# Optimization experiments

Hardware: AMD Instinct MI355X
Metric: run time of the kernel (lower is better)

The kernel has to match this reference:

```python
import jax, jax.numpy as jnp
import numpy as np

N_HEADS = 16


def setup_inputs() -> dict:
    key = jax.random.key(0)
    k1, k2, k3, k4 = jax.random.split(key, 4)
    b, s, d = 2, 2048, 1024
    x = jax.random.normal(k1, (b, s, d), dtype=jnp.float32)
    attn_B = jax.random.normal(k2, (b, N_HEADS, s, s), dtype=jnp.float32) * 0.02
    W_attn = jax.random.normal(k3, (d, 3 * d), dtype=jnp.float32) * (1.0 / np.sqrt(d))
    b_attn = jax.random.normal(k4, (3 * d,), dtype=jnp.float32) * 0.01
    return {"x": x, "attn_B": attn_B, "W_attn": W_attn, "b_attn": b_attn}


def reference(x, attn_B, W_attn, b_attn):
    b, s, d = x.shape
    h = N_HEADS
    hd = d // h
    qkv = x @ W_attn + b_attn                       # [b, s, 3d]
    Q, K, V = jnp.split(qkv, 3, axis=-1)
    # [b, s, d] -> [b, h, s, hd]
    Q = Q.reshape(b, s, h, hd).transpose(0, 2, 1, 3)
    K = K.reshape(b, s, h, hd).transpose(0, 2, 1, 3)
    V = V.reshape(b, s, h, hd).transpose(0, 2, 1, 3)
    scale = 1.0 / jnp.sqrt(jnp.asarray(hd, dtype=Q.dtype))
    scores = jnp.einsum("bhqk,bhsk->bhqs", Q, K) * scale   # [b, h, s, s]
    attn = jax.nn.softmax(scores, axis=-1) + attn_B          # post-softmax additive bias
    y = jnp.einsum("bhqs,bhsd->bhqd", attn, V)               # [b, h, s, hd]
    y = y.transpose(0, 2, 1, 3).reshape(b, s, d)
    return y
```

## Files before the change

### kernel.cpp

```cpp
#include <hip/hip_runtime.h>
#include <hip/hip_bf16.h>


typedef __attribute__((ext_vector_type(4))) float  f32x4;
typedef __attribute__((ext_vector_type(8))) short  bf16x8;
typedef __attribute__((ext_vector_type(4))) short  s16x4;
typedef __attribute__((ext_vector_type(4))) unsigned u32x4;

__device__ __forceinline__ short f2bf(float f) {
    __hip_bfloat16 h = __float2bfloat16(f);
    return __builtin_bit_cast(short, h);
}

__device__ __forceinline__ unsigned cvt_pk_bf16(float lo, float hi) {
    unsigned w;
    asm("v_cvt_pk_bf16_f32 %0, %1, %2" : "=v"(w) : "v"(lo), "v"(hi));
    return w;
}

__device__ __forceinline__ bf16x8 pack8(f32x4 a, f32x4 b) {
    u32x4 t = (u32x4){cvt_pk_bf16(a[0], a[1]), cvt_pk_bf16(a[2], a[3]),
                      cvt_pk_bf16(b[0], b[1]), cvt_pk_bf16(b[2], b[3])};
    return __builtin_bit_cast(bf16x8, t);
}

__device__ __forceinline__ void gll16(const short* g, short* l) {
    __builtin_amdgcn_global_load_lds(
        (const __attribute__((address_space(1))) void*)g,
        (__attribute__((address_space(3))) void*)l, 16, 0, 0);
}

__global__ void conv_x_kernel(const float* __restrict__ x, short* __restrict__ xb) {
    int idx = blockIdx.x * 256 + threadIdx.x;
    f32x4 v = *reinterpret_cast<const f32x4*>(x + (size_t)idx * 4);
    s16x4 o;
    o[0] = f2bf(v[0]); o[1] = f2bf(v[1]); o[2] = f2bf(v[2]); o[3] = f2bf(v[3]);
    *reinterpret_cast<s16x4*>(xb + (size_t)idx * 4) = o;
}

__global__ void wtrans_kernel(const float* __restrict__ W, short* __restrict__ Wt) {
    __shared__ float tile[64][65];
    int kb = blockIdx.x, nb = blockIdx.y;
    int t = threadIdx.x;
    int c4 = (t & 15) * 4;
    int r0 = t >> 4;
#pragma unroll
    for (int rr = 0; rr < 4; ++rr) {
        int kl = r0 + rr * 16;
        f32x4 v = *reinterpret_cast<const f32x4*>(W + (size_t)(kb * 64 + kl) * 3072 + nb * 64 + c4);
        tile[kl][c4 + 0] = v[0]; tile[kl][c4 + 1] = v[1];
        tile[kl][c4 + 2] = v[2]; tile[kl][c4 + 3] = v[3];
    }
    __syncthreads();
#pragma unroll
    for (int rr = 0; rr < 4; ++rr) {
        int nl = r0 + rr * 16;
        s16x4 o;
#pragma unroll
        for (int i = 0; i < 4; ++i) o[i] = f2bf(tile[c4 + i][nl]);
        *reinterpret_cast<s16x4*>(Wt + (size_t)(nb * 64 + nl) * 1024 + kb * 64 + c4) = o;
    }
}

__global__ __launch_bounds__(256) void qkv_gemm_kernel(
    const short* __restrict__ xb, const short* __restrict__ Wt,
    const float* __restrict__ bias,
    short* __restrict__ Qo, short* __restrict__ Ko, short* __restrict__ Vto)
{
    __shared__ short As[128 * 64];
    __shared__ short Bs[128 * 64];
    int tid = threadIdx.x;
    int wave = tid >> 6, lane = tid & 63, g = lane >> 4, lr = lane & 15;
    int wr = wave >> 1, wc = wave & 1;
    int bm = blockIdx.x, bn = blockIdx.y;

    f32x4 acc[4][4];
#pragma unroll
    for (int a = 0; a < 4; ++a)
#pragma unroll
        for (int b = 0; b < 4; ++b) acc[a][b] = (f32x4){0.f, 0.f, 0.f, 0.f};

    for (int k0 = 0; k0 < 1024; k0 += 64) {
#pragma unroll
        for (int j = 0; j < 4; ++j) {
            int c = j * 256 + tid;
            int row = c >> 3, cc = c & 7;
            int scc = (cc ^ (row & 7)) * 8;
            gll16(xb + (size_t)(bm * 128 + row) * 1024 + k0 + scc,
                  &As[(j * 256 + wave * 64) * 8]);
            gll16(Wt + (size_t)(bn * 128 + row) * 1024 + k0 + scc,
                  &Bs[(j * 256 + wave * 64) * 8]);
        }
        __syncthreads();

        bf16x8 af[2][4], bfr[2][4];
#pragma unroll
        for (int mt = 0; mt < 4; ++mt) {
            int row = wr * 64 + mt * 16 + lr;
            af[0][mt] = *reinterpret_cast<const bf16x8*>(&As[row * 64 + (((g    ) ^ (lr & 7)) * 8)]);
            af[1][mt] = *reinterpret_cast<const bf16x8*>(&As[row * 64 + (((g + 4) ^ (lr & 7)) * 8)]);
        }
#pragma unroll
        for (int nt = 0; nt < 4; ++nt) {
            int row = wc * 64 + nt * 16 + lr;
            bfr[0][nt] = *reinterpret_cast<const bf16x8*>(&Bs[row * 64 + (((g    ) ^ (lr & 7)) * 8)]);
            bfr[1][nt] = *reinterpret_cast<const bf16x8*>(&Bs[row * 64 + (((g + 4) ^ (lr & 7)) * 8)]);
        }
#pragma unroll
        for (int mt = 0; mt < 4; ++mt)
#pragma unroll
            for (int nt = 0; nt < 4; ++nt) {
                acc[mt][nt] = __builtin_amdgcn_mfma_f32_16x16x32_bf16(af[0][mt], bfr[0][nt], acc[mt][nt], 0, 0, 0);
                acc[mt][nt] = __builtin_amdgcn_mfma_f32_16x16x32_bf16(af[1][mt], bfr[1][nt], acc[mt][nt], 0, 0, 0);
            }
        __syncthreads();
    }

#pragma unroll
    for (int nt = 0; nt < 4; ++nt) {
        int n = bn * 128 + wc * 64 + nt * 16 + lr;
        float bv = bias[n];
        int which = n >> 10;
        int h = (n >> 6) & 15;
        int dd = n & 63;
#pragma unroll
        for (int mt = 0; mt < 4; ++mt) {
            int m0 = bm * 128 + wr * 64 + mt * 16 + g * 4;
            int bb = m0 >> 11, s0 = m0 & 2047;
            if (which == 2) {
                s16x4 o;
#pragma unroll
                for (int r = 0; r < 4; ++r) o[r] = f2bf(acc[mt][nt][r] + bv);
                *reinterpret_cast<s16x4*>(
                    Vto + ((size_t)(bb * 16 + h) * 64 + dd) * 2048 + s0) = o;
            } else {
                short* base = (which == 0) ? Qo : Ko;
#pragma unroll
                for (int r = 0; r < 4; ++r)
                    base[(((size_t)bb * 16 + h) * 2048 + s0 + r) * 64 + dd] =
                        f2bf(acc[mt][nt][r] + bv);
            }
        }
    }
}

__global__ __launch_bounds__(512, 4) void attn_kernel(
    const short* __restrict__ Qw, const short* __restrict__ Kw, const short* __restrict__ Vtw,
    const float* __restrict__ attnB, float* __restrict__ out)
{
    __shared__ short Ks [2][64 * 64];
    __shared__ short Vts[2][64 * 64];
    __shared__ short Ps [8][16 * 64];

    int id = blockIdx.x;
    int bh3 = id & 7;
    int qt  = (id >> 3) & 15;
    int bh  = ((id >> 7) << 3) | bh3;
    int b = bh >> 4, h = bh & 15;
    int tid = threadIdx.x;
    int wave = tid >> 6, lane = tid & 63, g = lane >> 4, lr = lane & 15;

    const short* Qb = Qw  + (size_t)bh * 2048 * 64;
    const short* Kb = Kw  + (size_t)bh * 2048 * 64;
    const short* Vb = Vtw + (size_t)bh * 64 * 2048;
    const float* Bp = attnB + (size_t)bh * 2048 * 2048;

    int qbase = qt * 128 + wave * 16;

    bf16x8 qf0, qf1;
    {
        const short* qp = Qb + (size_t)(qbase + lr) * 64 + g * 8;
        qf0 = *reinterpret_cast<const bf16x8*>(qp);
        qf1 = *reinterpret_cast<const bf16x8*>(qp + 32);
    }
    const float* brow = Bp + (size_t)(qbase + lr) * 2048 + g * 8;

    f32x4 Os[4], Ob[4];
#pragma unroll
    for (int dt = 0; dt < 4; ++dt) { Os[dt] = (f32x4){0.f,0.f,0.f,0.f}; Ob[dt] = (f32x4){0.f,0.f,0.f,0.f}; }
    float lsum = 0.f;

#define STAGE_KV(buf, ktt) do {                                                   \
    int row = tid >> 3, cc = tid & 7;                                             \
    int scc = (cc ^ (row & 7)) * 8;                                               \
    gll16(Kb + (size_t)((ktt) * 64 + row) * 64 + scc,                             \
          &Ks[buf][wave * 512]);                                                  \
    gll16(Vb + (size_t)row * 2048 + (ktt) * 64 + scc,                             \
          &Vts[buf][wave * 512]);                                                 \
} while (0)

#define LOADB(d0, d1, d2, d3, ktt) do {                                           \
    const float* bp_ = brow + (size_t)(ktt) * 64;                                 \
    d0 = *reinterpret_cast<const f32x4*>(bp_);                                    \
    d1 = *reinterpret_cast<const f32x4*>(bp_ + 4);                                \
    d2 = *reinterpret_cast<const f32x4*>(bp_ + 32);                               \
    d3 = *reinterpret_cast<const f32x4*>(bp_ + 36);                               \
} while (0)

#define COMPUTE(cur, xb0, xb1) do {                                               \
    f32x4 S[4];                                                                   \
    __builtin_amdgcn_s_setprio(1);                                                \
    _Pragma("unroll")                                                             \
    for (int nt = 0; nt < 4; ++nt) {                                              \
        int row = nt * 16 + lr;                                                   \
        bf16x8 kf0 = *reinterpret_cast<const bf16x8*>(&Ks[cur][row * 64 + (((g    ) ^ (lr & 7)) * 8)]); \
        bf16x8 kf1 = *reinterpret_cast<const bf16x8*>(&Ks[cur][row * 64 + (((g + 4) ^ (lr & 7)) * 8)]); \
        f32x4 s = (f32x4){0.f,0.f,0.f,0.f};                                       \
        s = __builtin_amdgcn_mfma_f32_16x16x32_bf16(kf0, qf0, s, 0, 0, 0);        \
        s = __builtin_amdgcn_mfma_f32_16x16x32_bf16(kf1, qf1, s, 0, 0, 0);        \
        S[nt] = s;                                                                \
    }                                                                             \
    __builtin_amdgcn_s_setprio(0);                                                \
    _Pragma("unroll")                                                             \
    for (int nt = 0; nt < 4; ++nt)                                                \
        _Pragma("unroll")                                                         \
        for (int r = 0; r < 4; ++r) {                                             \
            float p = exp2f(S[nt][r] * 0.1803368801111f);                         \
            S[nt][r] = p;                                                         \
            lsum += p;                                                            \
        }                                                                         \
    short* psw = &Ps[wave][lr * 64];                                              \
    _Pragma("unroll")                                                             \
    for (int nt = 0; nt < 4; ++nt)                                                \
        _Pragma("unroll")                                                         \
        for (int rp = 0; rp < 2; ++rp) {                                          \
            unsigned w = cvt_pk_bf16(S[nt][2 * rp], S[nt][2 * rp + 1]);           \
            int kp = 8 * nt + 2 * g + rp;                                         \
            int bi = kp >> 2, off = kp & 3;                                       \
            *reinterpret_cast<unsigned*>(psw + ((bi ^ (lr & 7)) << 3) + off * 2) = w; \
        }                                                                         \
    bf16x8 pf0 = *reinterpret_cast<const bf16x8*>(&Ps[wave][lr * 64 + (((g    ) ^ (lr & 7)) * 8)]); \
    bf16x8 pf1 = *reinterpret_cast<const bf16x8*>(&Ps[wave][lr * 64 + (((g + 4) ^ (lr & 7)) * 8)]); \
    __builtin_amdgcn_s_setprio(1);                                                \
    _Pragma("unroll")                                                             \
    for (int dt = 0; dt < 4; ++dt) {                                              \
        int row = dt * 16 + lr;                                                   \
        bf16x8 v0 = *reinterpret_cast<const bf16x8*>(&Vts[cur][row * 64 + (((g    ) ^ (lr & 7)) * 8)]); \
        bf16x8 v1 = *reinterpret_cast<const bf16x8*>(&Vts[cur][row * 64 + (((g + 4) ^ (lr & 7)) * 8)]); \
        Os[dt] = __builtin_amdgcn_mfma_f32_16x16x32_bf16(pf0, v0, Os[dt], 0, 0, 0); \
        Os[dt] = __builtin_amdgcn_mfma_f32_16x16x32_bf16(pf1, v1, Os[dt], 0, 0, 0); \
        Ob[dt] = __builtin_amdgcn_mfma_f32_16x16x32_bf16(xb0, v0, Ob[dt], 0, 0, 0); \
        Ob[dt] = __builtin_amdgcn_mfma_f32_16x16x32_bf16(xb1, v1, Ob[dt], 0, 0, 0); \
    }                                                                             \
    __builtin_amdgcn_s_setprio(0);                                                \
} while (0)

    f32x4 a0, a1, a2, a3, p0, p1, p2, p3;

    STAGE_KV(0, 0);
    __builtin_amdgcn_sched_barrier(0);
    LOADB(a0, a1, a2, a3, 0);
    LOADB(p0, p1, p2, p3, 1);
    __builtin_amdgcn_sched_barrier(0);
    asm volatile("s_waitcnt vmcnt(8)" ::: "memory");
    __builtin_amdgcn_s_barrier();
    __builtin_amdgcn_sched_barrier(0);

    for (int t = 0; t < 16; ++t) {
        {
            bf16x8 bbf0 = pack8(a0, a1);
            bf16x8 bbf1 = pack8(a2, a3);
            STAGE_KV(1, 2 * t + 1);
            __builtin_amdgcn_sched_barrier(0);
            if (t < 15) LOADB(a0, a1, a2, a3, 2 * t + 2);
            __builtin_amdgcn_sched_barrier(0);
            COMPUTE(0, bbf0, bbf1);
            if (t < 15) {
                asm volatile("s_waitcnt vmcnt(4)" ::: "memory");
            } else {
                asm volatile("s_waitcnt vmcnt(0)" ::: "memory");
            }
            __builtin_amdgcn_s_barrier();
            __builtin_amdgcn_sched_barrier(0);
        }
        {
            bf16x8 bbf0 = pack8(p0, p1);
            bf16x8 bbf1 = pack8(p2, p3);
            if (t < 15) {
                STAGE_KV(0, 2 * t + 2);
                __builtin_amdgcn_sched_barrier(0);
                LOADB(p0, p1, p2, p3, 2 * t + 3);
                __builtin_amdgcn_sched_barrier(0);
            }
            COMPUTE(1, bbf0, bbf1);
            if (t < 15) {
                asm volatile("s_waitcnt vmcnt(4)" ::: "memory");
                __builtin_amdgcn_s_barrier();
                __builtin_amdgcn_sched_barrier(0);
            }
        }
    }
#undef STAGE_KV
#undef LOADB
#undef COMPUTE

    float l = lsum;
    l += __shfl_xor(l, 16);
    l += __shfl_xor(l, 32);
    float inv = 1.0f / l;
#pragma unroll
    for (int r = 0; r < 4; ++r) {
        float invr = __shfl(inv, g * 4 + r);
        int q = qbase + g * 4 + r;
#pragma unroll
        for (int dt = 0; dt < 4; ++dt) {
            int dcol = dt * 16 + lr;
            float v = Os[dt][r] * invr + Ob[dt][r];
            __builtin_nontemporal_store(v, &out[((size_t)(b * 2048 + q) * 16 + h) * 64 + dcol]);
        }
    }
}

extern "C" void kernel_launch(void* const* d_in, const int* in_sizes, int n_in,
                              void* d_out, int out_size, void* d_ws, size_t ws_size,
                              hipStream_t stream) {
    const float* x     = (const float*)d_in[0];
    const float* attnB = (const float*)d_in[1];
    const float* W     = (const float*)d_in[2];
    const float* bias  = (const float*)d_in[3];
    float* out = (float*)d_out;

    short* ws = (short*)d_ws;
    short* xb = ws;
    short* Wt = xb + 4194304;
    short* Q  = Wt + 3145728;
    short* K  = Q  + 4194304;
    short* Vt = K  + 4194304;

    conv_x_kernel<<<4096, 256, 0, stream>>>(x, xb);
    wtrans_kernel<<<dim3(16, 48), 256, 0, stream>>>(W, Wt);
    qkv_gemm_kernel<<<dim3(32, 24), 256, 0, stream>>>(xb, Wt, bias, Q, K, Vt);
    attn_kernel<<<512, 512, 0, stream>>>(Q, K, Vt, attnB, out);
}
```

Before: 208.1 us.

## Rework QKV GEMM into 256x256 tiles with 4-stage async LDS pipeline

The QKV projection GEMM moves from 128x128 tiles and single-buffered 64-wide K steps to 256x256 tiles with 512 threads, 32-wide K steps and a 4-deep ring of LDS buffers. Global-to-LDS loads run three stages ahead, with explicit vmcnt waits and one barrier per step. The block order is remapped across XCDs, and setprio is raised around the MFMA burst. The aim is to hide load latency and raise arithmetic intensity. The cost is 192 blocks (fewer than the CU count), so some CUs may sit idle, and register pressure is higher.

```diff
diff --git a/kernel.cpp b/kernel.cpp
--- a/kernel.cpp
+++ b/kernel.cpp
@@ -62,75 +62,102 @@
     }
 }
 
-__global__ __launch_bounds__(256) void qkv_gemm_kernel(
+__global__ __launch_bounds__(512, 2) void qkv_gemm_kernel(
     const short* __restrict__ xb, const short* __restrict__ Wt,
     const float* __restrict__ bias,
     short* __restrict__ Qo, short* __restrict__ Ko, short* __restrict__ Vto)
 {
-    __shared__ short As[128 * 64];
-    __shared__ short Bs[128 * 64];
+    __shared__ short As[4][256 * 32];
+    __shared__ short Bs[4][256 * 32];
+
+    int id = blockIdx.x;
+    int wg = (id & 7) * 24 + (id >> 3);
+    int bm = wg & 15;
+    int bn = wg >> 4;
+
     int tid = threadIdx.x;
     int wave = tid >> 6, lane = tid & 63, g = lane >> 4, lr = lane & 15;
-    int wr = wave >> 1, wc = wave & 1;
-    int bm = blockIdx.x, bn = blockIdx.y;
-
-    f32x4 acc[4][4];
-#pragma unroll
-    for (int a = 0; a < 4; ++a)
-#pragma unroll
-        for (int b = 0; b < 4; ++b) acc[a][b] = (f32x4){0.f, 0.f, 0.f, 0.f};
-
-    for (int k0 = 0; k0 < 1024; k0 += 64) {
-#pragma unroll
-        for (int j = 0; j < 4; ++j) {
-            int c = j * 256 + tid;
-            int row = c >> 3, cc = c & 7;
-            int scc = (cc ^ (row & 7)) * 8;
-            gll16(xb + (size_t)(bm * 128 + row) * 1024 + k0 + scc,
-                  &As[(j * 256 + wave * 64) * 8]);
-            gll16(Wt + (size_t)(bn * 128 + row) * 1024 + k0 + scc,
-                  &Bs[(j * 256 + wave * 64) * 8]);
-        }
-        __syncthreads();
-
-        bf16x8 af[2][4], bfr[2][4];
-#pragma unroll
-        for (int mt = 0; mt < 4; ++mt) {
-            int row = wr * 64 + mt * 16 + lr;
-            af[0][mt] = *reinterpret_cast<const bf16x8*>(&As[row * 64 + (((g    ) ^ (lr & 7)) * 8)]);
-            af[1][mt] = *reinterpret_cast<const bf16x8*>(&As[row * 64 + (((g + 4) ^ (lr & 7)) * 8)]);
-        }
-#pragma unroll
-        for (int nt = 0; nt < 4; ++nt) {
-            int row = wc * 64 + nt * 16 + lr;
-            bfr[0][nt] = *reinterpret_cast<const bf16x8*>(&Bs[row * 64 + (((g    ) ^ (lr & 7)) * 8)]);
-            bfr[1][nt] = *reinterpret_cast<const bf16x8*>(&Bs[row * 64 + (((g + 4) ^ (lr & 7)) * 8)]);
-        }
-#pragma unroll
-        for (int mt = 0; mt < 4; ++mt)
-#pragma unroll
-            for (int nt = 0; nt < 4; ++nt) {
-                acc[mt][nt] = __builtin_amdgcn_mfma_f32_16x16x32_bf16(af[0][mt], bfr[0][nt], acc[mt][nt], 0, 0, 0);
-                acc[mt][nt] = __builtin_amdgcn_mfma_f32_16x16x32_bf16(af[1][mt], bfr[1][nt], acc[mt][nt], 0, 0, 0);
-            }
-        __syncthreads();
-    }
-
-#pragma unroll
-    for (int nt = 0; nt < 4; ++nt) {
-        int n = bn * 128 + wc * 64 + nt * 16 + lr;
-        float bv = bias[n];
-        int which = n >> 10;
-        int h = (n >> 6) & 15;
-        int dd = n & 63;
-#pragma unroll
-        for (int mt = 0; mt < 4; ++mt) {
-            int m0 = bm * 128 + wr * 64 + mt * 16 + g * 4;
+    int wr = wave >> 2, wc = wave & 3;
+
+    f32x4 acc[8][4];
+#pragma unroll
+    for (int m = 0; m < 8; ++m)
+#pragma unroll
+        for (int n = 0; n < 4; ++n) acc[m][n] = (f32x4){0.f, 0.f, 0.f, 0.f};
+
+#define STAGE(buf, tt) do {                                                       \
+    _Pragma("unroll")                                                             \
+    for (int j = 0; j < 2; ++j) {                                                 \
+        int c = j * 512 + tid;                      \
+        int row = c >> 2, ch = c & 3;                                             \
+        int scc = (ch ^ ((row + (row >> 2)) & 3)) * 8;                            \
+        gll16(xb + (size_t)(bm * 256 + row) * 1024 + (tt) * 32 + scc,             \
+              &As[buf][(j * 512 + wave * 64) * 8]);                               \
+        gll16(Wt + (size_t)(bn * 256 + row) * 1024 + (tt) * 32 + scc,             \
+              &Bs[buf][(j * 512 + wave * 64) * 8]);                               \
+    }                                                                             \
+} while (0)
+
+    STAGE(0, 0);
+    STAGE(1, 1);
+    STAGE(2, 2);
+    __builtin_amdgcn_sched_barrier(0);
+    asm volatile("s_waitcnt vmcnt(8)" ::: "memory");
+    __builtin_amdgcn_s_barrier();
+    __builtin_amdgcn_sched_barrier(0);
+
+    for (int t = 0; t < 32; ++t) {
+        int buf = t & 3;
+        if (t <= 28) STAGE((t + 3) & 3, t + 3);
+        __builtin_amdgcn_sched_barrier(0);
+
+        bf16x8 a[8], bq[4];
+#pragma unroll
+        for (int m = 0; m < 8; ++m) {
+            int row = wr * 128 + m * 16 + lr;
+            a[m] = *reinterpret_cast<const bf16x8*>(
+                &As[buf][row * 32 + ((g ^ ((row + (row >> 2)) & 3)) * 8)]);
+        }
+#pragma unroll
+        for (int n = 0; n < 4; ++n) {
+            int row = wc * 64 + n * 16 + lr;
+            bq[n] = *reinterpret_cast<const bf16x8*>(
+                &Bs[buf][row * 32 + ((g ^ ((row + (row >> 2)) & 3)) * 8)]);
+        }
+
+        __builtin_amdgcn_s_setprio(1);
+#pragma unroll
+        for (int m = 0; m < 8; ++m)
+#pragma unroll
+            for (int n = 0; n < 4; ++n)
+                acc[m][n] = __builtin_amdgcn_mfma_f32_16x16x32_bf16(a[m], bq[n], acc[m][n], 0, 0, 0);
+        __builtin_amdgcn_s_setprio(0);
+
+        if (t <= 28)      { asm volatile("s_waitcnt vmcnt(8)" ::: "memory"); }
+        else if (t == 29) { asm volatile("s_waitcnt vmcnt(4)" ::: "memory"); }
+        else if (t == 30) { asm volatile("s_waitcnt vmcnt(0)" ::: "memory"); }
+        if (t < 31) {
+            __builtin_amdgcn_s_barrier();
+            __builtin_amdgcn_sched_barrier(0);
+        }
+    }
+#undef STAGE
+
+#pragma unroll
+    for (int n = 0; n < 4; ++n) {
+        int ncol = bn * 256 + wc * 64 + n * 16 + lr;
+        float bv = bias[ncol];
+        int which = ncol >> 10;
+        int h = (ncol >> 6) & 15;
+        int dd = ncol & 63;
+#pragma unroll
+        for (int m = 0; m < 8; ++m) {
+            int m0 = bm * 256 + wr * 128 + m * 16 + g * 4;
             int bb = m0 >> 11, s0 = m0 & 2047;
             if (which == 2) {
                 s16x4 o;
 #pragma unroll
-                for (int r = 0; r < 4; ++r) o[r] = f2bf(acc[mt][nt][r] + bv);
+                for (int r = 0; r < 4; ++r) o[r] = f2bf(acc[m][n][r] + bv);
                 *reinterpret_cast<s16x4*>(
                     Vto + ((size_t)(bb * 16 + h) * 64 + dd) * 2048 + s0) = o;
             } else {
@@ -138,7 +165,7 @@
 #pragma unroll
                 for (int r = 0; r < 4; ++r)
                     base[(((size_t)bb * 16 + h) * 2048 + s0 + r) * 64 + dd] =
-                        f2bf(acc[mt][nt][r] + bv);
+                        f2bf(acc[m][n][r] + bv);
             }
         }
     }
@@ -329,6 +356,6 @@
 
     conv_x_kernel<<<4096, 256, 0, stream>>>(x, xb);
     wtrans_kernel<<<dim3(16, 48), 256, 0, stream>>>(W, Wt);
-    qkv_gemm_kernel<<<dim3(32, 24), 256, 0, stream>>>(xb, Wt, bias, Q, K, Vt);
+    qkv_gemm_kernel<<<192, 512, 0, stream>>>(xb, Wt, bias, Q, K, Vt);
     attn_kernel<<<512, 512, 0, stream>>>(Q, K, Vt, attnB, out);
 }
```

Measured after the change: 218.2 us. +4.9%, slower.
